# Performance work log

Hardware: AMD Instinct MI355X
Metric: run time of the kernel (lower is better)

## Reference

```python
import jax, jax.numpy as jnp
import numpy as np

D_IN = 5
H = 512

def _init_params(key):
    ks = jax.random.split(key, 10)
    s1 = 1.0 / np.sqrt(H)
    u = lambda k, shape: jax.random.uniform(k, shape, jnp.float32, -s1, s1)
    return dict(
        W_ih1=u(ks[0], (4 * H, D_IN)), W_hh1=u(ks[1], (4 * H, H)),
        b_ih1=u(ks[2], (4 * H,)), b_hh1=u(ks[3], (4 * H,)),
        W_ih2=u(ks[4], (4 * H, H)), W_hh2=u(ks[5], (4 * H, H)),
        b_ih2=u(ks[6], (4 * H,)), b_hh2=u(ks[7], (4 * H,)),
        W_lin=u(ks[8], (1, H)), b_lin=u(ks[9], (1,)),
    )

def setup_inputs() -> dict:
    key = jax.random.key(0)
    kx, kp = jax.random.split(key)
    T, B = 512, 128
    inp = {"x": jax.random.normal(kx, (T, B, D_IN), dtype=jnp.float32)}
    inp.update(_init_params(kp))
    return inp

def _lstm_cell(x, h, c, W_ih, W_hh, b_ih, b_hh):
    # gates: [B, 4H], PyTorch gate order i, f, g, o
    gates = x @ W_ih.T + b_ih + h @ W_hh.T + b_hh
    i, f, g, o = jnp.split(gates, 4, axis=-1)
    c_new = jax.nn.sigmoid(f) * c + jax.nn.sigmoid(i) * jnp.tanh(g)
    h_new = jax.nn.sigmoid(o) * jnp.tanh(c_new)
    return h_new, c_new

def reference(x, W_ih1, W_hh1, b_ih1, b_hh1, W_ih2, W_hh2, b_ih2, b_hh2, W_lin, b_lin):
    B = x.shape[1]
    z = jnp.zeros((B, H), dtype=x.dtype)

    def step(carry, x_t):
        h1, c1, h2, c2 = carry
        h1, c1 = _lstm_cell(x_t, h1, c1, W_ih1, W_hh1, b_ih1, b_hh1)
        h2, c2 = _lstm_cell(h1, h2, c2, W_ih2, W_hh2, b_ih2, b_hh2)
        out = h2 @ W_lin.T + b_lin  # [B, 1]
        return (h1, c1, h2, c2), out[:, 0]

    _, ys = jax.lax.scan(step, (z, z, z, z), x)  # ys: [T, B]
    return ys.T  # [B, T] == torch.stack(outputs, 1).squeeze(2)
```

## Files before the change

### kernel.cpp

```cpp
#include <hip/hip_runtime.h>
#include <hip/hip_fp16.h>


#define HDIM   512
#define TSTEPS 512
#define BATCH  128
#define DIN    5
#define NGRP   4
#define MGRP   32
#define NB1    16
#define NB2    32
#define RING   16

#define OFF_W1 0u
#define OFF_W2 2097152u
#define OFF_H1 6291456u
#define OFF_H2 8388608u
#define OFF_F1 8650752u
#define OFF_F2 8675328u
#define WS_END 8699904u

typedef _Float16 half8 __attribute__((ext_vector_type(8)));
typedef float    floatx4 __attribute__((ext_vector_type(4)));
typedef unsigned long long u64;

__device__ __forceinline__ float sigf(float v) { return 1.0f / (1.0f + __expf(-v)); }

__device__ __forceinline__ half8 as_h8(uint4 u) {
  union { uint4 u; half8 h; } c; c.u = u; return c.h;
}
__device__ __forceinline__ void ring_st8(_Float16* p, u64 v) {
  __hip_atomic_store((u64*)p, v, __ATOMIC_RELAXED, __HIP_MEMORY_SCOPE_AGENT);
}
__device__ __forceinline__ void lda16(const _Float16* p, uint4* a) {
  asm volatile(
      "global_load_dwordx4 %0, %16, off sc0 sc1\n\t"
      "global_load_dwordx4 %1, %16, off offset:64 sc0 sc1\n\t"
      "global_load_dwordx4 %2, %16, off offset:128 sc0 sc1\n\t"
      "global_load_dwordx4 %3, %16, off offset:192 sc0 sc1\n\t"
      "global_load_dwordx4 %4, %16, off offset:256 sc0 sc1\n\t"
      "global_load_dwordx4 %5, %16, off offset:320 sc0 sc1\n\t"
      "global_load_dwordx4 %6, %16, off offset:384 sc0 sc1\n\t"
      "global_load_dwordx4 %7, %16, off offset:448 sc0 sc1\n\t"
      "global_load_dwordx4 %8, %16, off offset:512 sc0 sc1\n\t"
      "global_load_dwordx4 %9, %16, off offset:576 sc0 sc1\n\t"
      "global_load_dwordx4 %10, %16, off offset:640 sc0 sc1\n\t"
      "global_load_dwordx4 %11, %16, off offset:704 sc0 sc1\n\t"
      "global_load_dwordx4 %12, %16, off offset:768 sc0 sc1\n\t"
      "global_load_dwordx4 %13, %16, off offset:832 sc0 sc1\n\t"
      "global_load_dwordx4 %14, %16, off offset:896 sc0 sc1\n\t"
      "global_load_dwordx4 %15, %16, off offset:960 sc0 sc1\n\t"
      "s_waitcnt vmcnt(0)"
      : "=v"(a[0]), "=v"(a[1]), "=v"(a[2]), "=v"(a[3]),
        "=v"(a[4]), "=v"(a[5]), "=v"(a[6]), "=v"(a[7]),
        "=v"(a[8]), "=v"(a[9]), "=v"(a[10]), "=v"(a[11]),
        "=v"(a[12]), "=v"(a[13]), "=v"(a[14]), "=v"(a[15])
      : "v"(p)
      : "memory");
}
__device__ __forceinline__ void poll_line(const unsigned* line, int n, unsigned tgt,
                                          int lane) {
  for (;;) {
    unsigned v = tgt;
    if (lane < n)
      v = __hip_atomic_load(line + lane, __ATOMIC_RELAXED, __HIP_MEMORY_SCOPE_AGENT);
    if (__all((int)(v >= tgt))) break;
  }
  __asm__ __volatile__("" ::: "memory");
}

extern "C" __global__ void init_kernel(char* __restrict__ ws, float* __restrict__ out,
                                       const float* __restrict__ blin) {
  unsigned tid = blockIdx.x * 256u + threadIdx.x;
  unsigned nz = (WS_END - OFF_H1) / 16u;
  if (tid < nz) ((uint4*)(ws + OFF_H1))[tid] = make_uint4(0, 0, 0, 0);
  if (tid < (unsigned)(BATCH * TSTEPS)) out[tid] = blin[0];
}

extern "C" __global__ void pack_kernel(const float* __restrict__ Whh1,
                                       const float* __restrict__ Wih2,
                                       const float* __restrict__ Whh2,
                                       char* __restrict__ ws) {
  unsigned tid = blockIdx.x * 256u + threadIdx.x;
  const float* src;
  char* dst;
  if (tid < 131072u) {
    unsigned lane = tid & 63u, ks = (tid >> 6) & 15u, gg = (tid >> 10) & 3u,
             h = (tid >> 12) & 1u, j = tid >> 13;
    unsigned cg = j * 32u + h * 16u + (lane & 15u);
    unsigned row = gg * 512u + cg;
    unsigned k0 = ks * 32u + (lane >> 4) * 8u;
    src = Whh1 + (size_t)row * 512u + k0;
    dst = ws + OFF_W1 + (size_t)tid * 16u;
  } else {
    unsigned t2 = tid - 131072u;
    if (t2 >= 262144u) return;
    unsigned lane = t2 & 63u, ksl = (t2 >> 6) & 15u, gg = (t2 >> 10) & 3u,
             kh = (t2 >> 12) & 1u, j = t2 >> 13;
    unsigned cg = j * 16u + (lane & 15u);
    unsigned row = gg * 512u + cg;
    unsigned kp = kh * 512u + ksl * 32u + (lane >> 4) * 8u;
    src = (kp < 512u) ? (Wih2 + (size_t)row * 512u + kp)
                      : (Whh2 + (size_t)row * 512u + (kp - 512u));
    dst = ws + OFF_W2 + (size_t)t2 * 16u;
  }
  float4 lo = ((const float4*)src)[0];
  float4 hi = ((const float4*)src)[1];
  _Float16 v[8] = {(_Float16)lo.x, (_Float16)lo.y, (_Float16)lo.z, (_Float16)lo.w,
                   (_Float16)hi.x, (_Float16)hi.y, (_Float16)hi.z, (_Float16)hi.w};
  *(uint4*)dst = *(const uint4*)v;
}

extern "C" __global__ __launch_bounds__(256, 1) void lstm_persist(
    const float* __restrict__ x,
    const float* __restrict__ Wih1,
    const float* __restrict__ bih1, const float* __restrict__ bhh1,
    const float* __restrict__ bih2, const float* __restrict__ bhh2,
    const float* __restrict__ Wlin,
    float* __restrict__ out,
    char* __restrict__ ws) {
  __shared__ char smem[16384];

  const int blk = blockIdx.x;
  const int xcd = blk & 7;
  const int slot = blk >> 3;
  const int tid = threadIdx.x;
  const int wave = tid >> 6;
  const int lane = tid & 63;
  const int nlane = lane & 15;
  const int quad = lane >> 4;

  _Float16* h1ring = (_Float16*)(ws + OFF_H1);
  _Float16* h2ring = (_Float16*)(ws + OFF_H2);

  if (xcd >= NGRP) {
    const int g = xcd - NGRP;
    const int j = slot;
    if (j >= NB1) return;
    const char* gW = ws + OFF_W1 + (size_t)j * 131072u;

    unsigned* f1g = (unsigned*)(ws + OFF_F1) + (size_t)g * 48 * 32;
    unsigned* f2g = (unsigned*)(ws + OFF_F2) + (size_t)g * 48 * 32;
    const unsigned* myline1 = f1g + (size_t)j * 32;
    const unsigned* mybp    = f2g + (size_t)(32 + j) * 32;
    _Float16* ring = h1ring + (size_t)g * (RING * MGRP * HDIM);
    _Float16* tile = (_Float16*)smem;

    const int mt = wave >> 1;
    const int hh = wave & 1;
    const int cg = j * 32 + hh * 16 + nlane;

    half8 breg[64];
#pragma unroll
    for (int r = 0; r < 64; ++r)
      breg[r] = *(const half8*)(gW + (size_t)((hh * 64 + r) * 64 + lane) * 16);

    float bias_r[4], wih[4][5];
    for (int gg = 0; gg < 4; ++gg) {
      int row = gg * 512 + cg;
      bias_r[gg] = bih1[row] + bhh1[row];
      for (int k = 0; k < 5; ++k) wih[gg][k] = Wih1[row * 5 + k];
    }
    float cstate[4] = {};

    for (int t = 0; t < TSTEPS; ++t) {
      if (t) poll_line(myline1, NB1, (unsigned)t, lane);
      if ((t & 7) == 0 && t >= 16) poll_line(mybp, NB2, (unsigned)(t - 8), lane);

      const _Float16* ap =
          ring + (size_t)((t + RING - 1) & (RING - 1)) * (MGRP * HDIM) +
          mt * 16 * HDIM + nlane * HDIM + quad * 8;
      uint4 areg[16];
      lda16(ap, areg);

      float xr[4][5];
#pragma unroll
      for (int r = 0; r < 4; ++r) {
        int b = g * MGRP + mt * 16 + quad * 4 + r;
        const float* xp = x + ((size_t)t * BATCH + b) * DIN;
#pragma unroll
        for (int k = 0; k < 5; ++k) xr[r][k] = xp[k];
      }
      floatx4 acc[4];
#pragma unroll
      for (int gg = 0; gg < 4; ++gg) {
#pragma unroll
        for (int r = 0; r < 4; ++r) {
          float s = bias_r[gg];
#pragma unroll
          for (int k = 0; k < 5; ++k) s += xr[r][k] * wih[gg][k];
          acc[gg][r] = s;
        }
      }
#pragma unroll
      for (int ks = 0; ks < 16; ++ks) {
        half8 av = as_h8(areg[ks]);
#pragma unroll
        for (int gg = 0; gg < 4; ++gg)
          acc[gg] = __builtin_amdgcn_mfma_f32_16x16x32_f16(av, breg[gg * 16 + ks],
                                                           acc[gg], 0, 0, 0);
      }
#pragma unroll
      for (int r = 0; r < 4; ++r) {
        float iv = acc[0][r], fv = acc[1][r], gv = acc[2][r], ov = acc[3][r];
        float cn = sigf(fv) * cstate[r] + sigf(iv) * tanhf(gv);
        float hn = sigf(ov) * tanhf(cn);
        cstate[r] = cn;
        tile[(mt * 16 + quad * 4 + r) * 32 + hh * 16 + nlane] = (_Float16)hn;
      }
      __syncthreads();
      {
        _Float16* hout = ring + (size_t)(t & (RING - 1)) * (MGRP * HDIM);
        u64 v = *(const u64*)(tile + (tid >> 3) * 32 + (tid & 7) * 4);
        ring_st8(hout + (tid >> 3) * HDIM + j * 32 + (tid & 7) * 4, v);
      }
      __syncthreads();
      if (tid < 48)
        __hip_atomic_fetch_add(f1g + (size_t)tid * 32 + j, 1u, __ATOMIC_RELAXED,
                               __HIP_MEMORY_SCOPE_AGENT);
    }
  } else {
    const int g = xcd;
    const int j = slot;
    const char* gW = ws + OFF_W2 + (size_t)j * 131072u;

    unsigned* f1g = (unsigned*)(ws + OFF_F1) + (size_t)g * 48 * 32;
    unsigned* f2g = (unsigned*)(ws + OFF_F2) + (size_t)g * 48 * 32;
    const unsigned* myline1 = f1g + (size_t)(16 + j) * 32;
    const unsigned* myline2 = f2g + (size_t)j * 32;
    const _Float16* h1rd = h1ring + (size_t)g * (RING * MGRP * HDIM);
    _Float16* ring2 = h2ring + (size_t)g * (2 * MGRP * HDIM);
    floatx4* pbase = (floatx4*)smem;
    _Float16* tile2 = (_Float16*)(smem + 8192);

    const int kh = wave & 1;
    const int mt = wave >> 1;
    const int cg = j * 16 + nlane;

    half8 breg[64];
#pragma unroll
    for (int r = 0; r < 64; ++r)
      breg[r] = *(const half8*)(gW + (size_t)((kh * 64 + r) * 64 + lane) * 16);

    float bias_r[4];
    for (int gg = 0; gg < 4; ++gg) {
      int row = gg * 512 + cg;
      bias_r[gg] = bih2[row] + bhh2[row];
    }
    const float wl = Wlin[cg];
    float cstate[4] = {};

    for (int t = 0; t < TSTEPS; ++t) {
      if (kh == 0) poll_line(myline1, NB1, (unsigned)(t + 1), lane);
      else if (t)  poll_line(myline2, NB2, (unsigned)t, lane);

      const _Float16* abase = (kh == 0)
          ? h1rd + (size_t)(t & (RING - 1)) * (MGRP * HDIM) + mt * 16 * HDIM +
                nlane * HDIM + quad * 8
          : ring2 + (size_t)((t + 1) & 1) * (MGRP * HDIM) + mt * 16 * HDIM +
                nlane * HDIM + quad * 8;
      uint4 areg[16];
      lda16(abase, areg);

      floatx4 acc[4];
#pragma unroll
      for (int gg = 0; gg < 4; ++gg)
        acc[gg] = (kh == 0)
            ? (floatx4){bias_r[gg], bias_r[gg], bias_r[gg], bias_r[gg]}
            : (floatx4){0.f, 0.f, 0.f, 0.f};
#pragma unroll
      for (int ks = 0; ks < 16; ++ks) {
        half8 av = as_h8(areg[ks]);
#pragma unroll
        for (int gg = 0; gg < 4; ++gg)
          acc[gg] = __builtin_amdgcn_mfma_f32_16x16x32_f16(av, breg[gg * 16 + ks],
                                                           acc[gg], 0, 0, 0);
      }
      if (kh == 1) {
#pragma unroll
        for (int gg = 0; gg < 4; ++gg) pbase[(mt * 4 + gg) * 64 + lane] = acc[gg];
      }
      __syncthreads();
      float red[4];
      if (kh == 0) {
#pragma unroll
        for (int gg = 0; gg < 4; ++gg) acc[gg] += pbase[(mt * 4 + gg) * 64 + lane];
#pragma unroll
        for (int r = 0; r < 4; ++r) {
          float iv = acc[0][r], fv = acc[1][r], gv = acc[2][r], ov = acc[3][r];
          float cn = sigf(fv) * cstate[r] + sigf(iv) * tanhf(gv);
          float hn = sigf(ov) * tanhf(cn);
          cstate[r] = cn;
          tile2[(mt * 16 + quad * 4 + r) * 16 + nlane] = (_Float16)hn;
          red[r] = wl * hn;
        }
      }
      __syncthreads();
      if (tid < 128) {
        u64 v = *(const u64*)(tile2 + (tid >> 2) * 16 + (tid & 3) * 4);
        ring_st8(ring2 + (size_t)(t & 1) * (MGRP * HDIM) + (tid >> 2) * HDIM +
                     j * 16 + (tid & 3) * 4, v);
      }
      __syncthreads();
      if (tid < 48)
        __hip_atomic_fetch_add(f2g + (size_t)tid * 32 + j, 1u, __ATOMIC_RELAXED,
                               __HIP_MEMORY_SCOPE_AGENT);
      if (kh == 0) {
#pragma unroll
        for (int r = 0; r < 4; ++r) {
          float v2 = red[r];
          v2 += __shfl_xor(v2, 1, 64);
          v2 += __shfl_xor(v2, 2, 64);
          v2 += __shfl_xor(v2, 4, 64);
          v2 += __shfl_xor(v2, 8, 64);
          red[r] = v2;
        }
        if (nlane == 0) {
#pragma unroll
          for (int r = 0; r < 4; ++r) {
            int b = g * MGRP + mt * 16 + quad * 4 + r;
            atomicAdd(out + (size_t)b * TSTEPS + t, red[r]);
          }
        }
      }
    }
  }
}

extern "C" void kernel_launch(void* const* d_in, const int* in_sizes, int n_in,
                              void* d_out, int out_size, void* d_ws, size_t ws_size,
                              hipStream_t stream) {
  const float* x    = (const float*)d_in[0];
  const float* Wih1 = (const float*)d_in[1];
  const float* Whh1 = (const float*)d_in[2];
  const float* bih1 = (const float*)d_in[3];
  const float* bhh1 = (const float*)d_in[4];
  const float* Wih2 = (const float*)d_in[5];
  const float* Whh2 = (const float*)d_in[6];
  const float* bih2 = (const float*)d_in[7];
  const float* bhh2 = (const float*)d_in[8];
  const float* Wlin = (const float*)d_in[9];
  const float* blin = (const float*)d_in[10];
  float* out = (float*)d_out;
  char* ws = (char*)d_ws;

  init_kernel<<<640, 256, 0, stream>>>(ws, out, blin);
  pack_kernel<<<1536, 256, 0, stream>>>(Whh1, Wih2, Whh2, ws);
  lstm_persist<<<256, 256, 0, stream>>>(x, Wih1, bih1, bhh1, bih2, bhh2, Wlin, out, ws);
}
```

Measured before the change: 2.318 ms.

## Split batch across all eight XCDs with per-XCC role assignment and blocked rings

Repartitions the persistent LSTM so that each of 8 XCC groups handles 16 batch rows, instead of 4 groups handling 32 rows with layers split across XCDs. Blocks read their hardware XCC id and take a role from an atomic counter, so that layer-1 and layer-2 producers and consumers share one XCC's L2. Ring layouts are made blocked per producer, loads drop sc1, and stores use atomic swaps followed by a flag increment from a single wave. The aim is to cut cross-XCD coherence latency on each timestep handoff. In exchange it adds a spin cap that could silently break ordering, and it depends on the occupancy of each XCC.

New measurement: 2.725 ms. 17.6% more time.

```diff
diff --git a/kernel.cpp b/kernel.cpp
--- a/kernel.cpp
+++ b/kernel.cpp
@@ -6,19 +6,19 @@
 #define TSTEPS 512
 #define BATCH  128
 #define DIN    5
-#define NGRP   4
-#define MGRP   32
-#define NB1    16
-#define NB2    32
+#define NGRP   8
+#define BROWS  16
+#define NB1    8
+#define NB2    16
 #define RING   16
-
-#define OFF_W1 0u
-#define OFF_W2 2097152u
-#define OFF_H1 6291456u
-#define OFF_H2 8388608u
-#define OFF_F1 8650752u
-#define OFF_F2 8675328u
-#define WS_END 8699904u
+#define SPIN_CAP 65536
+
+#define OFF_W1  0u
+#define OFF_W2  2097152u
+#define OFF_H1  6291456u
+#define OFF_H2  8388608u
+#define OFF_FL  8650752u
+#define WS_END  8699904u
 
 typedef _Float16 half8 __attribute__((ext_vector_type(8)));
 typedef float    floatx4 __attribute__((ext_vector_type(4)));
@@ -29,44 +29,92 @@
 __device__ __forceinline__ half8 as_h8(uint4 u) {
   union { uint4 u; half8 h; } c; c.u = u; return c.h;
 }
-__device__ __forceinline__ void ring_st8(_Float16* p, u64 v) {
-  __hip_atomic_store((u64*)p, v, __ATOMIC_RELAXED, __HIP_MEMORY_SCOPE_AGENT);
-}
-__device__ __forceinline__ void lda16(const _Float16* p, uint4* a) {
-  asm volatile(
-      "global_load_dwordx4 %0, %16, off sc0 sc1\n\t"
-      "global_load_dwordx4 %1, %16, off offset:64 sc0 sc1\n\t"
-      "global_load_dwordx4 %2, %16, off offset:128 sc0 sc1\n\t"
-      "global_load_dwordx4 %3, %16, off offset:192 sc0 sc1\n\t"
-      "global_load_dwordx4 %4, %16, off offset:256 sc0 sc1\n\t"
-      "global_load_dwordx4 %5, %16, off offset:320 sc0 sc1\n\t"
-      "global_load_dwordx4 %6, %16, off offset:384 sc0 sc1\n\t"
-      "global_load_dwordx4 %7, %16, off offset:448 sc0 sc1\n\t"
-      "global_load_dwordx4 %8, %16, off offset:512 sc0 sc1\n\t"
-      "global_load_dwordx4 %9, %16, off offset:576 sc0 sc1\n\t"
-      "global_load_dwordx4 %10, %16, off offset:640 sc0 sc1\n\t"
-      "global_load_dwordx4 %11, %16, off offset:704 sc0 sc1\n\t"
-      "global_load_dwordx4 %12, %16, off offset:768 sc0 sc1\n\t"
-      "global_load_dwordx4 %13, %16, off offset:832 sc0 sc1\n\t"
-      "global_load_dwordx4 %14, %16, off offset:896 sc0 sc1\n\t"
-      "global_load_dwordx4 %15, %16, off offset:960 sc0 sc1\n\t"
-      "s_waitcnt vmcnt(0)"
-      : "=v"(a[0]), "=v"(a[1]), "=v"(a[2]), "=v"(a[3]),
-        "=v"(a[4]), "=v"(a[5]), "=v"(a[6]), "=v"(a[7]),
-        "=v"(a[8]), "=v"(a[9]), "=v"(a[10]), "=v"(a[11]),
-        "=v"(a[12]), "=v"(a[13]), "=v"(a[14]), "=v"(a[15])
-      : "v"(p)
-      : "memory");
-}
+
+__device__ __forceinline__ unsigned ld_xcc() {
+  unsigned v;
+  asm volatile("s_getreg_b32 %0, hwreg(HW_REG_XCC_ID)" : "=s"(v));
+  return v & 7u;
+}
+
+__device__ __forceinline__ void st8_swap(_Float16* p, u64 v) {
+  asm volatile("global_atomic_swap_x2 %0, %1, off" :: "v"(p), "v"(v) : "memory");
+}
+
+__device__ __forceinline__ void flag_add(unsigned* p) {
+  __hip_atomic_fetch_add(p, 1u, __ATOMIC_RELAXED, __HIP_MEMORY_SCOPE_AGENT);
+}
+
 __device__ __forceinline__ void poll_line(const unsigned* line, int n, unsigned tgt,
                                           int lane) {
-  for (;;) {
+  for (int it = 0; it < SPIN_CAP; ++it) {
     unsigned v = tgt;
     if (lane < n)
       v = __hip_atomic_load(line + lane, __ATOMIC_RELAXED, __HIP_MEMORY_SCOPE_AGENT);
     if (__all((int)(v >= tgt))) break;
   }
   __asm__ __volatile__("" ::: "memory");
+}
+
+__device__ __forceinline__ void lda16a(const _Float16* b, uint4* a) {
+  const _Float16* b0 = b;
+  const _Float16* b1 = b + 2048;
+  const _Float16* b2 = b + 4096;
+  const _Float16* b3 = b + 6144;
+  asm volatile(
+      "global_load_dwordx4 %0, %16, off sc0\n\t"
+      "global_load_dwordx4 %1, %16, off offset:64 sc0\n\t"
+      "global_load_dwordx4 %2, %16, off offset:2048 sc0\n\t"
+      "global_load_dwordx4 %3, %16, off offset:2112 sc0\n\t"
+      "global_load_dwordx4 %4, %17, off sc0\n\t"
+      "global_load_dwordx4 %5, %17, off offset:64 sc0\n\t"
+      "global_load_dwordx4 %6, %17, off offset:2048 sc0\n\t"
+      "global_load_dwordx4 %7, %17, off offset:2112 sc0\n\t"
+      "global_load_dwordx4 %8, %18, off sc0\n\t"
+      "global_load_dwordx4 %9, %18, off offset:64 sc0\n\t"
+      "global_load_dwordx4 %10, %18, off offset:2048 sc0\n\t"
+      "global_load_dwordx4 %11, %18, off offset:2112 sc0\n\t"
+      "global_load_dwordx4 %12, %19, off sc0\n\t"
+      "global_load_dwordx4 %13, %19, off offset:64 sc0\n\t"
+      "global_load_dwordx4 %14, %19, off offset:2048 sc0\n\t"
+      "global_load_dwordx4 %15, %19, off offset:2112 sc0\n\t"
+      "s_waitcnt vmcnt(0)"
+      : "=&v"(a[0]), "=&v"(a[1]), "=&v"(a[2]), "=&v"(a[3]),
+        "=&v"(a[4]), "=&v"(a[5]), "=&v"(a[6]), "=&v"(a[7]),
+        "=&v"(a[8]), "=&v"(a[9]), "=&v"(a[10]), "=&v"(a[11]),
+        "=&v"(a[12]), "=&v"(a[13]), "=&v"(a[14]), "=&v"(a[15])
+      : "v"(b0), "v"(b1), "v"(b2), "v"(b3)
+      : "memory");
+}
+
+__device__ __forceinline__ void lda16b(const _Float16* b, uint4* a) {
+  const _Float16* b0 = b;
+  const _Float16* b1 = b + 2048;
+  const _Float16* b2 = b + 4096;
+  const _Float16* b3 = b + 6144;
+  asm volatile(
+      "global_load_dwordx4 %0, %16, off sc0\n\t"
+      "global_load_dwordx4 %1, %16, off offset:1024 sc0\n\t"
+      "global_load_dwordx4 %2, %16, off offset:2048 sc0\n\t"
+      "global_load_dwordx4 %3, %16, off offset:3072 sc0\n\t"
+      "global_load_dwordx4 %4, %17, off sc0\n\t"
+      "global_load_dwordx4 %5, %17, off offset:1024 sc0\n\t"
+      "global_load_dwordx4 %6, %17, off offset:2048 sc0\n\t"
+      "global_load_dwordx4 %7, %17, off offset:3072 sc0\n\t"
+      "global_load_dwordx4 %8, %18, off sc0\n\t"
+      "global_load_dwordx4 %9, %18, off offset:1024 sc0\n\t"
+      "global_load_dwordx4 %10, %18, off offset:2048 sc0\n\t"
+      "global_load_dwordx4 %11, %18, off offset:3072 sc0\n\t"
+      "global_load_dwordx4 %12, %19, off sc0\n\t"
+      "global_load_dwordx4 %13, %19, off offset:1024 sc0\n\t"
+      "global_load_dwordx4 %14, %19, off offset:2048 sc0\n\t"
+      "global_load_dwordx4 %15, %19, off offset:3072 sc0\n\t"
+      "s_waitcnt vmcnt(0)"
+      : "=&v"(a[0]), "=&v"(a[1]), "=&v"(a[2]), "=&v"(a[3]),
+        "=&v"(a[4]), "=&v"(a[5]), "=&v"(a[6]), "=&v"(a[7]),
+        "=&v"(a[8]), "=&v"(a[9]), "=&v"(a[10]), "=&v"(a[11]),
+        "=&v"(a[12]), "=&v"(a[13]), "=&v"(a[14]), "=&v"(a[15])
+      : "v"(b0), "v"(b1), "v"(b2), "v"(b3)
+      : "memory");
 }
 
 extern "C" __global__ void init_kernel(char* __restrict__ ws, float* __restrict__ out,
@@ -86,8 +134,8 @@
   char* dst;
   if (tid < 131072u) {
     unsigned lane = tid & 63u, ks = (tid >> 6) & 15u, gg = (tid >> 10) & 3u,
-             h = (tid >> 12) & 1u, j = tid >> 13;
-    unsigned cg = j * 32u + h * 16u + (lane & 15u);
+             ch = (tid >> 12) & 3u, j = tid >> 14;
+    unsigned cg = j * 64u + ch * 16u + (lane & 15u);
     unsigned row = gg * 512u + cg;
     unsigned k0 = ks * 32u + (lane >> 4) * 8u;
     src = Whh1 + (size_t)row * 512u + k0;
@@ -95,11 +143,12 @@
   } else {
     unsigned t2 = tid - 131072u;
     if (t2 >= 262144u) return;
-    unsigned lane = t2 & 63u, ksl = (t2 >> 6) & 15u, gg = (t2 >> 10) & 3u,
-             kh = (t2 >> 12) & 1u, j = t2 >> 13;
-    unsigned cg = j * 16u + (lane & 15u);
+    unsigned lane = t2 & 63u, ks = (t2 >> 6) & 15u, gg = (t2 >> 10) & 3u,
+             wv = (t2 >> 12) & 3u, j = t2 >> 14;
+    unsigned kh = wv & 1u, ch = wv >> 1;
+    unsigned cg = j * 32u + ch * 16u + (lane & 15u);
     unsigned row = gg * 512u + cg;
-    unsigned kp = kh * 512u + ksl * 32u + (lane >> 4) * 8u;
+    unsigned kp = kh * 512u + ks * 32u + (lane >> 4) * 8u;
     src = (kp < 512u) ? (Wih2 + (size_t)row * 512u + kp)
                       : (Whh2 + (size_t)row * 512u + (kp - 512u));
     dst = ws + OFF_W2 + (size_t)t2 * 16u;
@@ -120,66 +169,58 @@
     float* __restrict__ out,
     char* __restrict__ ws) {
   __shared__ char smem[16384];
-
-  const int blk = blockIdx.x;
-  const int xcd = blk & 7;
-  const int slot = blk >> 3;
+  __shared__ unsigned role_s;
+
+  const unsigned xcc = ld_xcc();
+  unsigned* fl = (unsigned*)(ws + OFF_FL) + (size_t)xcc * 48 * 32;
+  if (threadIdx.x == 0)
+    role_s = __hip_atomic_fetch_add(fl + 31, 1u, __ATOMIC_RELAXED,
+                                    __HIP_MEMORY_SCOPE_AGENT);
+  __syncthreads();
+  const unsigned role = role_s;
+  if (role >= (unsigned)(NB1 + NB2)) return;
+
+  const int g = (int)xcc;
   const int tid = threadIdx.x;
   const int wave = tid >> 6;
   const int lane = tid & 63;
   const int nlane = lane & 15;
   const int quad = lane >> 4;
 
-  _Float16* h1ring = (_Float16*)(ws + OFF_H1);
-  _Float16* h2ring = (_Float16*)(ws + OFF_H2);
-
-  if (xcd >= NGRP) {
-    const int g = xcd - NGRP;
-    const int j = slot;
-    if (j >= NB1) return;
-    const char* gW = ws + OFF_W1 + (size_t)j * 131072u;
-
-    unsigned* f1g = (unsigned*)(ws + OFF_F1) + (size_t)g * 48 * 32;
-    unsigned* f2g = (unsigned*)(ws + OFF_F2) + (size_t)g * 48 * 32;
-    const unsigned* myline1 = f1g + (size_t)j * 32;
-    const unsigned* mybp    = f2g + (size_t)(32 + j) * 32;
-    _Float16* ring = h1ring + (size_t)g * (RING * MGRP * HDIM);
+  _Float16* ring1 = (_Float16*)(ws + OFF_H1) + (size_t)g * (RING * 8192);
+  _Float16* ring2 = (_Float16*)(ws + OFF_H2) + (size_t)g * (2 * 8192);
+
+  if (role < NB1) {
+    const int j = (int)role;
+    const char* gW = ws + OFF_W1 + (size_t)j * 262144u;
+    const unsigned* myline = fl + (size_t)j * 32;
+    const unsigned* mybp = fl + (size_t)(40 + j) * 32;
     _Float16* tile = (_Float16*)smem;
 
-    const int mt = wave >> 1;
-    const int hh = wave & 1;
-    const int cg = j * 32 + hh * 16 + nlane;
+    const int ch = wave;
+    const int cg = j * 64 + ch * 16 + nlane;
 
     half8 breg[64];
 #pragma unroll
     for (int r = 0; r < 64; ++r)
-      breg[r] = *(const half8*)(gW + (size_t)((hh * 64 + r) * 64 + lane) * 16);
-
-    float bias_r[4], wih[4][5];
+      breg[r] = *(const half8*)(gW + (size_t)(ch * 64 + r) * 1024 + lane * 16);
+
+    float bias_r[4], wih[4][DIN];
     for (int gg = 0; gg < 4; ++gg) {
       int row = gg * 512 + cg;
       bias_r[gg] = bih1[row] + bhh1[row];
-      for (int k = 0; k < 5; ++k) wih[gg][k] = Wih1[row * 5 + k];
+      for (int k = 0; k < DIN; ++k) wih[gg][k] = Wih1[row * DIN + k];
     }
     float cstate[4] = {};
 
     for (int t = 0; t < TSTEPS; ++t) {
-      if (t) poll_line(myline1, NB1, (unsigned)t, lane);
-      if ((t & 7) == 0 && t >= 16) poll_line(mybp, NB2, (unsigned)(t - 8), lane);
-
-      const _Float16* ap =
-          ring + (size_t)((t + RING - 1) & (RING - 1)) * (MGRP * HDIM) +
-          mt * 16 * HDIM + nlane * HDIM + quad * 8;
-      uint4 areg[16];
-      lda16(ap, areg);
-
-      float xr[4][5];
+      float xr[4][DIN];
 #pragma unroll
       for (int r = 0; r < 4; ++r) {
-        int b = g * MGRP + mt * 16 + quad * 4 + r;
+        int b = g * BROWS + quad * 4 + r;
         const float* xp = x + ((size_t)t * BATCH + b) * DIN;
 #pragma unroll
-        for (int k = 0; k < 5; ++k) xr[r][k] = xp[k];
+        for (int k = 0; k < DIN; ++k) xr[r][k] = xp[k];
       }
       floatx4 acc[4];
 #pragma unroll
@@ -188,10 +229,18 @@
         for (int r = 0; r < 4; ++r) {
           float s = bias_r[gg];
 #pragma unroll
-          for (int k = 0; k < 5; ++k) s += xr[r][k] * wih[gg][k];
+          for (int k = 0; k < DIN; ++k) s += xr[r][k] * wih[gg][k];
           acc[gg][r] = s;
         }
       }
+      if (t) poll_line(myline, NB1, (unsigned)t, lane);
+      if ((t & 7) == 0 && t >= RING) poll_line(mybp, NB2, (unsigned)(t - 8), lane);
+
+      uint4 areg[16];
+      lda16a(ring1 + (size_t)((t + RING - 1) & (RING - 1)) * 8192 +
+                 nlane * 64 + quad * 8,
+             areg);
+
 #pragma unroll
       for (int ks = 0; ks < 16; ++ks) {
         half8 av = as_h8(areg[ks]);
@@ -206,41 +255,38 @@
         float cn = sigf(fv) * cstate[r] + sigf(iv) * tanhf(gv);
         float hn = sigf(ov) * tanhf(cn);
         cstate[r] = cn;
-        tile[(mt * 16 + quad * 4 + r) * 32 + hh * 16 + nlane] = (_Float16)hn;
+        tile[(quad * 4 + r) * 64 + ch * 16 + nlane] = (_Float16)hn;
       }
       __syncthreads();
-      {
-        _Float16* hout = ring + (size_t)(t & (RING - 1)) * (MGRP * HDIM);
-        u64 v = *(const u64*)(tile + (tid >> 3) * 32 + (tid & 7) * 4);
-        ring_st8(hout + (tid >> 3) * HDIM + j * 32 + (tid & 7) * 4, v);
-      }
-      __syncthreads();
-      if (tid < 48)
-        __hip_atomic_fetch_add(f1g + (size_t)tid * 32 + j, 1u, __ATOMIC_RELAXED,
-                               __HIP_MEMORY_SCOPE_AGENT);
+      if (wave == 0) {
+        const int row = lane >> 2, c16 = (lane & 3) * 16;
+        const u64* tp = (const u64*)(tile + row * 64 + c16);
+        _Float16* dp = ring1 + (size_t)(t & (RING - 1)) * 8192 + j * 1024 +
+                       row * 64 + c16;
+        st8_swap(dp,      tp[0]);
+        st8_swap(dp + 4,  tp[1]);
+        st8_swap(dp + 8,  tp[2]);
+        st8_swap(dp + 12, tp[3]);
+        asm volatile("s_waitcnt vmcnt(0)" ::: "memory");
+        if (lane < 24) flag_add(fl + (size_t)lane * 32 + j);
+      }
     }
   } else {
-    const int g = xcd;
-    const int j = slot;
-    const char* gW = ws + OFF_W2 + (size_t)j * 131072u;
-
-    unsigned* f1g = (unsigned*)(ws + OFF_F1) + (size_t)g * 48 * 32;
-    unsigned* f2g = (unsigned*)(ws + OFF_F2) + (size_t)g * 48 * 32;
-    const unsigned* myline1 = f1g + (size_t)(16 + j) * 32;
-    const unsigned* myline2 = f2g + (size_t)j * 32;
-    const _Float16* h1rd = h1ring + (size_t)g * (RING * MGRP * HDIM);
-    _Float16* ring2 = h2ring + (size_t)g * (2 * MGRP * HDIM);
+    const int j = (int)role - NB1;
+    const char* gW = ws + OFF_W2 + (size_t)j * 262144u;
+    const unsigned* l_h1 = fl + (size_t)(8 + j) * 32;
+    const unsigned* l_h2 = fl + (size_t)(24 + j) * 32;
     floatx4* pbase = (floatx4*)smem;
     _Float16* tile2 = (_Float16*)(smem + 8192);
 
     const int kh = wave & 1;
-    const int mt = wave >> 1;
-    const int cg = j * 16 + nlane;
+    const int ch = wave >> 1;
+    const int cg = j * 32 + ch * 16 + nlane;
 
     half8 breg[64];
 #pragma unroll
     for (int r = 0; r < 64; ++r)
-      breg[r] = *(const half8*)(gW + (size_t)((kh * 64 + r) * 64 + lane) * 16);
+      breg[r] = *(const half8*)(gW + (size_t)(wave * 64 + r) * 1024 + lane * 16);
 
     float bias_r[4];
     for (int gg = 0; gg < 4; ++gg) {
@@ -251,17 +297,16 @@
     float cstate[4] = {};
 
     for (int t = 0; t < TSTEPS; ++t) {
-      if (kh == 0) poll_line(myline1, NB1, (unsigned)(t + 1), lane);
-      else if (t)  poll_line(myline2, NB2, (unsigned)t, lane);
-
-      const _Float16* abase = (kh == 0)
-          ? h1rd + (size_t)(t & (RING - 1)) * (MGRP * HDIM) + mt * 16 * HDIM +
-                nlane * HDIM + quad * 8
-          : ring2 + (size_t)((t + 1) & 1) * (MGRP * HDIM) + mt * 16 * HDIM +
-                nlane * HDIM + quad * 8;
       uint4 areg[16];
-      lda16(abase, areg);
-
+      if (kh == 0) {
+        poll_line(l_h1, NB1, (unsigned)(t + 1), lane);
+        lda16a(ring1 + (size_t)(t & (RING - 1)) * 8192 + nlane * 64 + quad * 8,
+               areg);
+      } else {
+        if (t) poll_line(l_h2, NB2, (unsigned)t, lane);
+        lda16b(ring2 + (size_t)((t + 1) & 1) * 8192 + nlane * 32 + quad * 8,
+               areg);
+      }
       floatx4 acc[4];
 #pragma unroll
       for (int gg = 0; gg < 4; ++gg)
@@ -278,33 +323,33 @@
       }
       if (kh == 1) {
 #pragma unroll
-        for (int gg = 0; gg < 4; ++gg) pbase[(mt * 4 + gg) * 64 + lane] = acc[gg];
+        for (int gg = 0; gg < 4; ++gg) pbase[(ch * 4 + gg) * 64 + lane] = acc[gg];
       }
       __syncthreads();
       float red[4];
       if (kh == 0) {
 #pragma unroll
-        for (int gg = 0; gg < 4; ++gg) acc[gg] += pbase[(mt * 4 + gg) * 64 + lane];
+        for (int gg = 0; gg < 4; ++gg) acc[gg] += pbase[(ch * 4 + gg) * 64 + lane];
 #pragma unroll
         for (int r = 0; r < 4; ++r) {
           float iv = acc[0][r], fv = acc[1][r], gv = acc[2][r], ov = acc[3][r];
           float cn = sigf(fv) * cstate[r] + sigf(iv) * tanhf(gv);
           float hn = sigf(ov) * tanhf(cn);
           cstate[r] = cn;
-          tile2[(mt * 16 + quad * 4 + r) * 16 + nlane] = (_Float16)hn;
+          tile2[(quad * 4 + r) * 32 + ch * 16 + nlane] = (_Float16)hn;
           red[r] = wl * hn;
         }
       }
       __syncthreads();
-      if (tid < 128) {
-        u64 v = *(const u64*)(tile2 + (tid >> 2) * 16 + (tid & 3) * 4);
-        ring_st8(ring2 + (size_t)(t & 1) * (MGRP * HDIM) + (tid >> 2) * HDIM +
-                     j * 16 + (tid & 3) * 4, v);
-      }
-      __syncthreads();
-      if (tid < 48)
-        __hip_atomic_fetch_add(f2g + (size_t)tid * 32 + j, 1u, __ATOMIC_RELAXED,
-                               __HIP_MEMORY_SCOPE_AGENT);
+      if (wave == 0) {
+        const int row = lane >> 2, c8 = (lane & 3) * 8;
+        const u64* tp = (const u64*)(tile2 + row * 32 + c8);
+        _Float16* dp = ring2 + (size_t)(t & 1) * 8192 + j * 512 + row * 32 + c8;
+        st8_swap(dp,     tp[0]);
+        st8_swap(dp + 4, tp[1]);
+        asm volatile("s_waitcnt vmcnt(0)" ::: "memory");
+        if (lane < 24) flag_add(fl + (size_t)(24 + lane) * 32 + j);
+      }
       if (kh == 0) {
 #pragma unroll
         for (int r = 0; r < 4; ++r) {
@@ -318,7 +363,7 @@
         if (nlane == 0) {
 #pragma unroll
           for (int r = 0; r < 4; ++r) {
-            int b = g * MGRP + mt * 16 + quad * 4 + r;
+            int b = g * BROWS + quad * 4 + r;
             atomicAdd(out + (size_t)b * TSTEPS + t, red[r]);
           }
         }
@@ -346,5 +391,5 @@
 
   init_kernel<<<640, 256, 0, stream>>>(ws, out, blin);
   pack_kernel<<<1536, 256, 0, stream>>>(Whh1, Wih2, Whh2, ws);
-  lstm_persist<<<256, 256, 0, stream>>>(x, Wih1, bih1, bhh1, bih2, bhh2, Wlin, out, ws);
-}
+  lstm_persist<<<384, 256, 0, stream>>>(x, Wih1, bih1, bhh1, bih2, bhh2, Wlin, out, ws);
+}
```

## Replace broadcast flag lines with per-producer padded counters and bounded polling

Applied to the files above, without the earlier changes.

Each producer block now increments one counter in its own 64-byte slot instead of atomically bumping 48 replicated flag lines, and consumers poll the strided counters directly. This cuts the atomic traffic per step from 48 atomics to one. The input projection from x is moved ahead of the poll so its latency overlaps the wait. The spin loop is capped at a fixed iteration count, which could let a block proceed on stale data if a producer is slow. The inline-asm outputs are also marked early-clobber.

New measurement: 2.523 ms. 1.09x slower.

```diff
diff --git a/kernel.cpp b/kernel.cpp
--- a/kernel.cpp
+++ b/kernel.cpp
@@ -11,13 +11,13 @@
 #define NB1    16
 #define NB2    32
 #define RING   16
+#define SPIN_CAP 16384
 
 #define OFF_W1 0u
 #define OFF_W2 2097152u
 #define OFF_H1 6291456u
 #define OFF_H2 8388608u
-#define OFF_F1 8650752u
-#define OFF_F2 8675328u
+#define OFF_CT 8650752u
 #define WS_END 8699904u
 
 typedef _Float16 half8 __attribute__((ext_vector_type(8)));
@@ -31,6 +31,20 @@
 }
 __device__ __forceinline__ void ring_st8(_Float16* p, u64 v) {
   __hip_atomic_store((u64*)p, v, __ATOMIC_RELAXED, __HIP_MEMORY_SCOPE_AGENT);
+}
+__device__ __forceinline__ void flag_add(unsigned* p) {
+  __hip_atomic_fetch_add(p, 1u, __ATOMIC_RELAXED, __HIP_MEMORY_SCOPE_AGENT);
+}
+__device__ __forceinline__ void poll_ctrs(const unsigned* base, int n, unsigned tgt,
+                                          int lane) {
+  for (int it = 0; it < SPIN_CAP; ++it) {
+    unsigned v = tgt;
+    if (lane < n)
+      v = __hip_atomic_load(base + (size_t)lane * 16, __ATOMIC_RELAXED,
+                            __HIP_MEMORY_SCOPE_AGENT);
+    if (__all((int)(v >= tgt))) break;
+  }
+  __asm__ __volatile__("" ::: "memory");
 }
 __device__ __forceinline__ void lda16(const _Float16* p, uint4* a) {
   asm volatile(
@@ -51,22 +65,12 @@
       "global_load_dwordx4 %14, %16, off offset:896 sc0 sc1\n\t"
       "global_load_dwordx4 %15, %16, off offset:960 sc0 sc1\n\t"
       "s_waitcnt vmcnt(0)"
-      : "=v"(a[0]), "=v"(a[1]), "=v"(a[2]), "=v"(a[3]),
-        "=v"(a[4]), "=v"(a[5]), "=v"(a[6]), "=v"(a[7]),
-        "=v"(a[8]), "=v"(a[9]), "=v"(a[10]), "=v"(a[11]),
-        "=v"(a[12]), "=v"(a[13]), "=v"(a[14]), "=v"(a[15])
+      : "=&v"(a[0]), "=&v"(a[1]), "=&v"(a[2]), "=&v"(a[3]),
+        "=&v"(a[4]), "=&v"(a[5]), "=&v"(a[6]), "=&v"(a[7]),
+        "=&v"(a[8]), "=&v"(a[9]), "=&v"(a[10]), "=&v"(a[11]),
+        "=&v"(a[12]), "=&v"(a[13]), "=&v"(a[14]), "=&v"(a[15])
       : "v"(p)
       : "memory");
-}
-__device__ __forceinline__ void poll_line(const unsigned* line, int n, unsigned tgt,
-                                          int lane) {
-  for (;;) {
-    unsigned v = tgt;
-    if (lane < n)
-      v = __hip_atomic_load(line + lane, __ATOMIC_RELAXED, __HIP_MEMORY_SCOPE_AGENT);
-    if (__all((int)(v >= tgt))) break;
-  }
-  __asm__ __volatile__("" ::: "memory");
 }
 
 extern "C" __global__ void init_kernel(char* __restrict__ ws, float* __restrict__ out,
@@ -139,10 +143,9 @@
     if (j >= NB1) return;
     const char* gW = ws + OFF_W1 + (size_t)j * 131072u;
 
-    unsigned* f1g = (unsigned*)(ws + OFF_F1) + (size_t)g * 48 * 32;
-    unsigned* f2g = (unsigned*)(ws + OFF_F2) + (size_t)g * 48 * 32;
-    const unsigned* myline1 = f1g + (size_t)j * 32;
-    const unsigned* mybp    = f2g + (size_t)(32 + j) * 32;
+    unsigned* cbase = (unsigned*)(ws + OFF_CT) + (size_t)g * 1536;
+    const unsigned* ctL1 = cbase;
+    const unsigned* ctL2 = cbase + 256;
     _Float16* ring = h1ring + (size_t)g * (RING * MGRP * HDIM);
     _Float16* tile = (_Float16*)smem;
 
@@ -164,8 +167,27 @@
     float cstate[4] = {};
 
     for (int t = 0; t < TSTEPS; ++t) {
-      if (t) poll_line(myline1, NB1, (unsigned)t, lane);
-      if ((t & 7) == 0 && t >= 16) poll_line(mybp, NB2, (unsigned)(t - 8), lane);
+      float xr[4][5];
+#pragma unroll
+      for (int r = 0; r < 4; ++r) {
+        int b = g * MGRP + mt * 16 + quad * 4 + r;
+        const float* xp = x + ((size_t)t * BATCH + b) * DIN;
+#pragma unroll
+        for (int k = 0; k < 5; ++k) xr[r][k] = xp[k];
+      }
+      floatx4 acc[4];
+#pragma unroll
+      for (int gg = 0; gg < 4; ++gg) {
+#pragma unroll
+        for (int r = 0; r < 4; ++r) {
+          float s = bias_r[gg];
+#pragma unroll
+          for (int k = 0; k < 5; ++k) s += xr[r][k] * wih[gg][k];
+          acc[gg][r] = s;
+        }
+      }
+      if (t) poll_ctrs(ctL1, NB1, (unsigned)t, lane);
+      if ((t & 7) == 0 && t >= 16) poll_ctrs(ctL2, NB2, (unsigned)(t - 8), lane);
 
       const _Float16* ap =
           ring + (size_t)((t + RING - 1) & (RING - 1)) * (MGRP * HDIM) +
@@ -173,25 +195,6 @@
       uint4 areg[16];
       lda16(ap, areg);
 
-      float xr[4][5];
-#pragma unroll
-      for (int r = 0; r < 4; ++r) {
-        int b = g * MGRP + mt * 16 + quad * 4 + r;
-        const float* xp = x + ((size_t)t * BATCH + b) * DIN;
-#pragma unroll
-        for (int k = 0; k < 5; ++k) xr[r][k] = xp[k];
-      }
-      floatx4 acc[4];
-#pragma unroll
-      for (int gg = 0; gg < 4; ++gg) {
-#pragma unroll
-        for (int r = 0; r < 4; ++r) {
-          float s = bias_r[gg];
-#pragma unroll
-          for (int k = 0; k < 5; ++k) s += xr[r][k] * wih[gg][k];
-          acc[gg][r] = s;
-        }
-      }
 #pragma unroll
       for (int ks = 0; ks < 16; ++ks) {
         half8 av = as_h8(areg[ks]);
@@ -215,19 +218,16 @@
         ring_st8(hout + (tid >> 3) * HDIM + j * 32 + (tid & 7) * 4, v);
       }
       __syncthreads();
-      if (tid < 48)
-        __hip_atomic_fetch_add(f1g + (size_t)tid * 32 + j, 1u, __ATOMIC_RELAXED,
-                               __HIP_MEMORY_SCOPE_AGENT);
+      if (tid == 0) flag_add(cbase + (size_t)j * 16);
     }
   } else {
     const int g = xcd;
     const int j = slot;
     const char* gW = ws + OFF_W2 + (size_t)j * 131072u;
 
-    unsigned* f1g = (unsigned*)(ws + OFF_F1) + (size_t)g * 48 * 32;
-    unsigned* f2g = (unsigned*)(ws + OFF_F2) + (size_t)g * 48 * 32;
-    const unsigned* myline1 = f1g + (size_t)(16 + j) * 32;
-    const unsigned* myline2 = f2g + (size_t)j * 32;
+    unsigned* cbase = (unsigned*)(ws + OFF_CT) + (size_t)g * 1536;
+    const unsigned* ctL1 = cbase;
+    const unsigned* ctL2 = cbase + 256;
     const _Float16* h1rd = h1ring + (size_t)g * (RING * MGRP * HDIM);
     _Float16* ring2 = h2ring + (size_t)g * (2 * MGRP * HDIM);
     floatx4* pbase = (floatx4*)smem;
@@ -251,8 +251,8 @@
     float cstate[4] = {};
 
     for (int t = 0; t < TSTEPS; ++t) {
-      if (kh == 0) poll_line(myline1, NB1, (unsigned)(t + 1), lane);
-      else if (t)  poll_line(myline2, NB2, (unsigned)t, lane);
+      if (kh == 0) poll_ctrs(ctL1, NB1, (unsigned)(t + 1), lane);
+      else if (t)  poll_ctrs(ctL2, NB2, (unsigned)t, lane);
 
       const _Float16* abase = (kh == 0)
           ? h1rd + (size_t)(t & (RING - 1)) * (MGRP * HDIM) + mt * 16 * HDIM +
@@ -302,9 +302,7 @@
                      j * 16 + (tid & 3) * 4, v);
       }
       __syncthreads();
-      if (tid < 48)
-        __hip_atomic_fetch_add(f2g + (size_t)tid * 32 + j, 1u, __ATOMIC_RELAXED,
-                               __HIP_MEMORY_SCOPE_AGENT);
+      if (tid == 0) flag_add(cbase + (size_t)(256 + j * 16));
       if (kh == 0) {
 #pragma unroll
         for (int r = 0; r < 4; ++r) {
```

## Replace block barriers with LDS counters and transpose MFMA operands for direct stores

Applied to the files above, without the earlier changes.

Swaps the MFMA operand order so each lane holds four consecutive hidden units for one batch row, which lets every wave store its h slice to the global ring directly instead of staging it through an LDS tile. The __syncthreads barriers are replaced by LDS atomic counters: the last wave to finish a step publishes the cross-block flags, and layer-2 k-halves hand off partial sums through a double-buffered LDS region. The layer-1 input projection now runs as an extra MFMA with fp16 x and W_ih instead of scalar FMAs, and is issued before polling. Spin loops are capped at a fixed iteration count, which adds the risk of proceeding on stale data if a wait runs long, and fp16 input projection slightly lowers precision.

Measured after the change: 2.676 ms. +15.5%, slower.

```diff
diff --git a/kernel.cpp b/kernel.cpp
--- a/kernel.cpp
+++ b/kernel.cpp
@@ -11,6 +11,7 @@
 #define NB1    16
 #define NB2    32
 #define RING   16
+#define SPIN_CAP 16384
 
 #define OFF_W1 0u
 #define OFF_W2 2097152u
@@ -31,6 +32,31 @@
 }
 __device__ __forceinline__ void ring_st8(_Float16* p, u64 v) {
   __hip_atomic_store((u64*)p, v, __ATOMIC_RELAXED, __HIP_MEMORY_SCOPE_AGENT);
+}
+__device__ __forceinline__ void flag_add(unsigned* p) {
+  __hip_atomic_fetch_add(p, 1u, __ATOMIC_RELAXED, __HIP_MEMORY_SCOPE_AGENT);
+}
+__device__ __forceinline__ void poll_line(const unsigned* line, int n, unsigned tgt,
+                                          int lane) {
+  for (int it = 0; it < SPIN_CAP; ++it) {
+    unsigned v = tgt;
+    if (lane < n)
+      v = __hip_atomic_load(line + lane, __ATOMIC_RELAXED, __HIP_MEMORY_SCOPE_AGENT);
+    if (__all((int)(v >= tgt))) break;
+  }
+  __asm__ __volatile__("" ::: "memory");
+}
+__device__ __forceinline__ unsigned lds_add(unsigned* p) {
+  return __hip_atomic_fetch_add(p, 1u, __ATOMIC_RELAXED, __HIP_MEMORY_SCOPE_WORKGROUP);
+}
+__device__ __forceinline__ unsigned lds_ld(const unsigned* p) {
+  return __hip_atomic_load(p, __ATOMIC_RELAXED, __HIP_MEMORY_SCOPE_WORKGROUP);
+}
+__device__ __forceinline__ void lds_wait2(const unsigned* a, const unsigned* b,
+                                          unsigned tgt) {
+  for (int it = 0; it < SPIN_CAP; ++it)
+    if (lds_ld(a) >= tgt && lds_ld(b) >= tgt) break;
+  __asm__ __volatile__("" ::: "memory");
 }
 __device__ __forceinline__ void lda16(const _Float16* p, uint4* a) {
   asm volatile(
@@ -51,22 +77,12 @@
       "global_load_dwordx4 %14, %16, off offset:896 sc0 sc1\n\t"
       "global_load_dwordx4 %15, %16, off offset:960 sc0 sc1\n\t"
       "s_waitcnt vmcnt(0)"
-      : "=v"(a[0]), "=v"(a[1]), "=v"(a[2]), "=v"(a[3]),
-        "=v"(a[4]), "=v"(a[5]), "=v"(a[6]), "=v"(a[7]),
-        "=v"(a[8]), "=v"(a[9]), "=v"(a[10]), "=v"(a[11]),
-        "=v"(a[12]), "=v"(a[13]), "=v"(a[14]), "=v"(a[15])
+      : "=&v"(a[0]), "=&v"(a[1]), "=&v"(a[2]), "=&v"(a[3]),
+        "=&v"(a[4]), "=&v"(a[5]), "=&v"(a[6]), "=&v"(a[7]),
+        "=&v"(a[8]), "=&v"(a[9]), "=&v"(a[10]), "=&v"(a[11]),
+        "=&v"(a[12]), "=&v"(a[13]), "=&v"(a[14]), "=&v"(a[15])
       : "v"(p)
       : "memory");
-}
-__device__ __forceinline__ void poll_line(const unsigned* line, int n, unsigned tgt,
-                                          int lane) {
-  for (;;) {
-    unsigned v = tgt;
-    if (lane < n)
-      v = __hip_atomic_load(line + lane, __ATOMIC_RELAXED, __HIP_MEMORY_SCOPE_AGENT);
-    if (__all((int)(v >= tgt))) break;
-  }
-  __asm__ __volatile__("" ::: "memory");
 }
 
 extern "C" __global__ void init_kernel(char* __restrict__ ws, float* __restrict__ out,
@@ -119,7 +135,8 @@
     const float* __restrict__ Wlin,
     float* __restrict__ out,
     char* __restrict__ ws) {
-  __shared__ char smem[16384];
+  __shared__ char smem[16512];
+  unsigned* cnt = (unsigned*)(smem + 16384);
 
   const int blk = blockIdx.x;
   const int xcd = blk & 7;
@@ -137,34 +154,63 @@
     const int g = xcd - NGRP;
     const int j = slot;
     if (j >= NB1) return;
+    if (tid < 16) cnt[tid] = 0;
+    __syncthreads();
     const char* gW = ws + OFF_W1 + (size_t)j * 131072u;
 
     unsigned* f1g = (unsigned*)(ws + OFF_F1) + (size_t)g * 48 * 32;
     unsigned* f2g = (unsigned*)(ws + OFF_F2) + (size_t)g * 48 * 32;
-    const unsigned* myline1 = f1g + (size_t)j * 32;
+    const unsigned* myline = f1g + (size_t)j * 32;
     const unsigned* mybp    = f2g + (size_t)(32 + j) * 32;
     _Float16* ring = h1ring + (size_t)g * (RING * MGRP * HDIM);
-    _Float16* tile = (_Float16*)smem;
 
     const int mt = wave >> 1;
     const int hh = wave & 1;
-    const int cg = j * 32 + hh * 16 + nlane;
 
     half8 breg[64];
 #pragma unroll
     for (int r = 0; r < 64; ++r)
       breg[r] = *(const half8*)(gW + (size_t)((hh * 64 + r) * 64 + lane) * 16);
 
-    float bias_r[4], wih[4][5];
+    float bias16[4][4];
+    half8 wfrag[4];
+#pragma unroll
     for (int gg = 0; gg < 4; ++gg) {
-      int row = gg * 512 + cg;
-      bias_r[gg] = bih1[row] + bhh1[row];
-      for (int k = 0; k < 5; ++k) wih[gg][k] = Wih1[row * 5 + k];
+#pragma unroll
+      for (int r = 0; r < 4; ++r) {
+        int col = j * 32 + hh * 16 + quad * 4 + r;
+        int row = gg * 512 + col;
+        bias16[gg][r] = bih1[row] + bhh1[row];
+      }
+      union { _Float16 e[8]; half8 v; } w;
+#pragma unroll
+      for (int k = 0; k < 8; ++k) w.e[k] = (_Float16)0.0f;
+      if (quad == 0) {
+        int col = j * 32 + hh * 16 + nlane;
+        const float* wp = Wih1 + (size_t)(gg * 512 + col) * DIN;
+#pragma unroll
+        for (int k = 0; k < DIN; ++k) w.e[k] = (_Float16)wp[k];
+      }
+      wfrag[gg] = w.v;
     }
     float cstate[4] = {};
+    const int xrow = g * MGRP + mt * 16 + nlane;
 
     for (int t = 0; t < TSTEPS; ++t) {
-      if (t) poll_line(myline1, NB1, (unsigned)t, lane);
+      union { _Float16 e[8]; half8 v; } xf;
+#pragma unroll
+      for (int k = 0; k < 8; ++k) xf.e[k] = (_Float16)0.0f;
+      if (quad == 0) {
+        const float* xp = x + ((size_t)t * BATCH + xrow) * DIN;
+#pragma unroll
+        for (int k = 0; k < DIN; ++k) xf.e[k] = (_Float16)xp[k];
+      }
+      floatx4 acc[4];
+#pragma unroll
+      for (int gg = 0; gg < 4; ++gg)
+        acc[gg] = (floatx4){bias16[gg][0], bias16[gg][1], bias16[gg][2],
+                            bias16[gg][3]};
+      if (t) poll_line(myline, NB1, (unsigned)t, lane);
       if ((t & 7) == 0 && t >= 16) poll_line(mybp, NB2, (unsigned)(t - 8), lane);
 
       const _Float16* ap =
@@ -173,154 +219,150 @@
       uint4 areg[16];
       lda16(ap, areg);
 
-      float xr[4][5];
-#pragma unroll
-      for (int r = 0; r < 4; ++r) {
-        int b = g * MGRP + mt * 16 + quad * 4 + r;
-        const float* xp = x + ((size_t)t * BATCH + b) * DIN;
-#pragma unroll
-        for (int k = 0; k < 5; ++k) xr[r][k] = xp[k];
-      }
-      floatx4 acc[4];
-#pragma unroll
-      for (int gg = 0; gg < 4; ++gg) {
-#pragma unroll
-        for (int r = 0; r < 4; ++r) {
-          float s = bias_r[gg];
-#pragma unroll
-          for (int k = 0; k < 5; ++k) s += xr[r][k] * wih[gg][k];
-          acc[gg][r] = s;
-        }
-      }
+#pragma unroll
+      for (int gg = 0; gg < 4; ++gg)
+        acc[gg] = __builtin_amdgcn_mfma_f32_16x16x32_f16(wfrag[gg], xf.v,
+                                                         acc[gg], 0, 0, 0);
 #pragma unroll
       for (int ks = 0; ks < 16; ++ks) {
         half8 av = as_h8(areg[ks]);
 #pragma unroll
         for (int gg = 0; gg < 4; ++gg)
-          acc[gg] = __builtin_amdgcn_mfma_f32_16x16x32_f16(av, breg[gg * 16 + ks],
+          acc[gg] = __builtin_amdgcn_mfma_f32_16x16x32_f16(breg[gg * 16 + ks], av,
                                                            acc[gg], 0, 0, 0);
       }
+      union { _Float16 h4[4]; u64 v; } hv;
 #pragma unroll
       for (int r = 0; r < 4; ++r) {
         float iv = acc[0][r], fv = acc[1][r], gv = acc[2][r], ov = acc[3][r];
         float cn = sigf(fv) * cstate[r] + sigf(iv) * tanhf(gv);
         float hn = sigf(ov) * tanhf(cn);
         cstate[r] = cn;
-        tile[(mt * 16 + quad * 4 + r) * 32 + hh * 16 + nlane] = (_Float16)hn;
-      }
-      __syncthreads();
-      {
-        _Float16* hout = ring + (size_t)(t & (RING - 1)) * (MGRP * HDIM);
-        u64 v = *(const u64*)(tile + (tid >> 3) * 32 + (tid & 7) * 4);
-        ring_st8(hout + (tid >> 3) * HDIM + j * 32 + (tid & 7) * 4, v);
-      }
-      __syncthreads();
-      if (tid < 48)
-        __hip_atomic_fetch_add(f1g + (size_t)tid * 32 + j, 1u, __ATOMIC_RELAXED,
-                               __HIP_MEMORY_SCOPE_AGENT);
+        hv.h4[r] = (_Float16)hn;
+      }
+      ring_st8(ring + (size_t)(t & (RING - 1)) * (MGRP * HDIM) +
+                   (size_t)(mt * 16 + nlane) * HDIM + j * 32 + hh * 16 + quad * 4,
+               hv.v);
+      asm volatile("s_waitcnt vmcnt(0)" ::: "memory");
+      unsigned old = 0;
+      if (lane == 0) old = lds_add(cnt);
+      old = __shfl(old, 0, 64);
+      if ((int)old == 4 * t + 3 && lane < 48)
+        flag_add(f1g + (size_t)lane * 32 + j);
     }
   } else {
     const int g = xcd;
     const int j = slot;
+    if (tid < 16) cnt[tid] = 0;
+    __syncthreads();
     const char* gW = ws + OFF_W2 + (size_t)j * 131072u;
 
     unsigned* f1g = (unsigned*)(ws + OFF_F1) + (size_t)g * 48 * 32;
     unsigned* f2g = (unsigned*)(ws + OFF_F2) + (size_t)g * 48 * 32;
-    const unsigned* myline1 = f1g + (size_t)(16 + j) * 32;
-    const unsigned* myline2 = f2g + (size_t)j * 32;
+    const unsigned* l_h1 = f1g + (size_t)(16 + j) * 32;
+    const unsigned* l_h2 = f2g + (size_t)j * 32;
     const _Float16* h1rd = h1ring + (size_t)g * (RING * MGRP * HDIM);
     _Float16* ring2 = h2ring + (size_t)g * (2 * MGRP * HDIM);
-    floatx4* pbase = (floatx4*)smem;
-    _Float16* tile2 = (_Float16*)(smem + 8192);
+    floatx4* pb = (floatx4*)smem;
 
     const int kh = wave & 1;
     const int mt = wave >> 1;
-    const int cg = j * 16 + nlane;
 
     half8 breg[64];
 #pragma unroll
     for (int r = 0; r < 64; ++r)
       breg[r] = *(const half8*)(gW + (size_t)((kh * 64 + r) * 64 + lane) * 16);
 
-    float bias_r[4];
-    for (int gg = 0; gg < 4; ++gg) {
-      int row = gg * 512 + cg;
-      bias_r[gg] = bih2[row] + bhh2[row];
-    }
-    const float wl = Wlin[cg];
+    float bias16[4][4];
+#pragma unroll
+    for (int gg = 0; gg < 4; ++gg)
+#pragma unroll
+      for (int r = 0; r < 4; ++r) {
+        int col = j * 16 + quad * 4 + r;
+        bias16[gg][r] = bih2[gg * 512 + col] + bhh2[gg * 512 + col];
+      }
+    float wl4[4];
+#pragma unroll
+    for (int r = 0; r < 4; ++r) wl4[r] = Wlin[j * 16 + quad * 4 + r];
     float cstate[4] = {};
 
-    for (int t = 0; t < TSTEPS; ++t) {
-      if (kh == 0) poll_line(myline1, NB1, (unsigned)(t + 1), lane);
-      else if (t)  poll_line(myline2, NB2, (unsigned)t, lane);
-
-      const _Float16* abase = (kh == 0)
-          ? h1rd + (size_t)(t & (RING - 1)) * (MGRP * HDIM) + mt * 16 * HDIM +
-                nlane * HDIM + quad * 8
-          : ring2 + (size_t)((t + 1) & 1) * (MGRP * HDIM) + mt * 16 * HDIM +
-                nlane * HDIM + quad * 8;
-      uint4 areg[16];
-      lda16(abase, areg);
-
-      floatx4 acc[4];
-#pragma unroll
-      for (int gg = 0; gg < 4; ++gg)
-        acc[gg] = (kh == 0)
-            ? (floatx4){bias_r[gg], bias_r[gg], bias_r[gg], bias_r[gg]}
-            : (floatx4){0.f, 0.f, 0.f, 0.f};
-#pragma unroll
-      for (int ks = 0; ks < 16; ++ks) {
-        half8 av = as_h8(areg[ks]);
+    if (kh == 0) {
+      for (int t = 0; t < TSTEPS; ++t) {
+        poll_line(l_h1, NB1, (unsigned)(t + 1), lane);
+        const _Float16* ap = h1rd + (size_t)(t & (RING - 1)) * (MGRP * HDIM) +
+                             mt * 16 * HDIM + nlane * HDIM + quad * 8;
+        uint4 areg[16];
+        lda16(ap, areg);
+        floatx4 acc[4];
 #pragma unroll
         for (int gg = 0; gg < 4; ++gg)
-          acc[gg] = __builtin_amdgcn_mfma_f32_16x16x32_f16(av, breg[gg * 16 + ks],
-                                                           acc[gg], 0, 0, 0);
-      }
-      if (kh == 1) {
-#pragma unroll
-        for (int gg = 0; gg < 4; ++gg) pbase[(mt * 4 + gg) * 64 + lane] = acc[gg];
-      }
-      __syncthreads();
-      float red[4];
-      if (kh == 0) {
-#pragma unroll
-        for (int gg = 0; gg < 4; ++gg) acc[gg] += pbase[(mt * 4 + gg) * 64 + lane];
+          acc[gg] = (floatx4){bias16[gg][0], bias16[gg][1], bias16[gg][2],
+                              bias16[gg][3]};
+#pragma unroll
+        for (int ks = 0; ks < 16; ++ks) {
+          half8 av = as_h8(areg[ks]);
+#pragma unroll
+          for (int gg = 0; gg < 4; ++gg)
+            acc[gg] = __builtin_amdgcn_mfma_f32_16x16x32_f16(breg[gg * 16 + ks],
+                                                             av, acc[gg], 0, 0, 0);
+        }
+        if (t >= 2) lds_wait2(cnt + 3, cnt + 4, (unsigned)(t - 1));
+#pragma unroll
+        for (int gg = 0; gg < 4; ++gg)
+          pb[(size_t)(t & 1) * 512 + (mt * 4 + gg) * 64 + lane] = acc[gg];
+        asm volatile("s_waitcnt lgkmcnt(0)" ::: "memory");
+        if (lane == 0) lds_add(cnt + 1 + mt);
+      }
+    } else {
+      for (int t = 0; t < TSTEPS; ++t) {
+        if (t) poll_line(l_h2, NB2, (unsigned)t, lane);
+        const _Float16* ap = ring2 + (size_t)((t + 1) & 1) * (MGRP * HDIM) +
+                             mt * 16 * HDIM + nlane * HDIM + quad * 8;
+        uint4 areg[16];
+        lda16(ap, areg);
+        floatx4 acc[4] = {{0.f, 0.f, 0.f, 0.f},
+                          {0.f, 0.f, 0.f, 0.f},
+                          {0.f, 0.f, 0.f, 0.f},
+                          {0.f, 0.f, 0.f, 0.f}};
+#pragma unroll
+        for (int ks = 0; ks < 16; ++ks) {
+          half8 av = as_h8(areg[ks]);
+#pragma unroll
+          for (int gg = 0; gg < 4; ++gg)
+            acc[gg] = __builtin_amdgcn_mfma_f32_16x16x32_f16(breg[gg * 16 + ks],
+                                                             av, acc[gg], 0, 0, 0);
+        }
+        lds_wait2(cnt + 1, cnt + 2, (unsigned)(t + 1));
+#pragma unroll
+        for (int gg = 0; gg < 4; ++gg)
+          acc[gg] += pb[(size_t)(t & 1) * 512 + (mt * 4 + gg) * 64 + lane];
+        asm volatile("s_waitcnt lgkmcnt(0)" ::: "memory");
+        if (lane == 0) lds_add(cnt + 3 + mt);
+        union { _Float16 h4[4]; u64 v; } hv;
+        float s = 0.f;
 #pragma unroll
         for (int r = 0; r < 4; ++r) {
           float iv = acc[0][r], fv = acc[1][r], gv = acc[2][r], ov = acc[3][r];
           float cn = sigf(fv) * cstate[r] + sigf(iv) * tanhf(gv);
           float hn = sigf(ov) * tanhf(cn);
           cstate[r] = cn;
-          tile2[(mt * 16 + quad * 4 + r) * 16 + nlane] = (_Float16)hn;
-          red[r] = wl * hn;
+          hv.h4[r] = (_Float16)hn;
+          s += wl4[r] * hn;
         }
-      }
-      __syncthreads();
-      if (tid < 128) {
-        u64 v = *(const u64*)(tile2 + (tid >> 2) * 16 + (tid & 3) * 4);
-        ring_st8(ring2 + (size_t)(t & 1) * (MGRP * HDIM) + (tid >> 2) * HDIM +
-                     j * 16 + (tid & 3) * 4, v);
-      }
-      __syncthreads();
-      if (tid < 48)
-        __hip_atomic_fetch_add(f2g + (size_t)tid * 32 + j, 1u, __ATOMIC_RELAXED,
-                               __HIP_MEMORY_SCOPE_AGENT);
-      if (kh == 0) {
-#pragma unroll
-        for (int r = 0; r < 4; ++r) {
-          float v2 = red[r];
-          v2 += __shfl_xor(v2, 1, 64);
-          v2 += __shfl_xor(v2, 2, 64);
-          v2 += __shfl_xor(v2, 4, 64);
-          v2 += __shfl_xor(v2, 8, 64);
-          red[r] = v2;
-        }
-        if (nlane == 0) {
-#pragma unroll
-          for (int r = 0; r < 4; ++r) {
-            int b = g * MGRP + mt * 16 + quad * 4 + r;
-            atomicAdd(out + (size_t)b * TSTEPS + t, red[r]);
-          }
+        ring_st8(ring2 + (size_t)(t & 1) * (MGRP * HDIM) +
+                     (size_t)(mt * 16 + nlane) * HDIM + j * 16 + quad * 4,
+                 hv.v);
+        asm volatile("s_waitcnt vmcnt(0)" ::: "memory");
+        unsigned old = 0;
+        if (lane == 0) old = lds_add(cnt);
+        old = __shfl(old, 0, 64);
+        if ((int)old == 2 * t + 1 && lane < 48)
+          flag_add(f2g + (size_t)lane * 32 + j);
+        s += __shfl_xor(s, 16, 64);
+        s += __shfl_xor(s, 32, 64);
+        if (quad == 0) {
+          int b = g * MGRP + mt * 16 + nlane;
+          atomicAdd(out + (size_t)b * TSTEPS + t, s);
         }
       }
     }
```
